# Kernel optimization log

Hardware: AMD Instinct MI355X
Metric: run time of the kernel (lower is better)

Reference implementation:

```python
import jax, jax.numpy as jnp
import numpy as np

N, E = 50000, 800000
IN, OUT = 128, 64  # in_channels, out_channels


def _w(key, fan_in, fan_out):
    return jax.random.normal(key, (fan_in, fan_out), dtype=jnp.float32) * (1.0 / np.sqrt(fan_in))


def setup_inputs() -> dict:
    key = jax.random.key(0)
    ks = jax.random.split(key, 16)
    x = jax.random.normal(ks[0], (N, IN), dtype=jnp.float32)
    edge_index = jax.random.randint(ks[1], (2, E), 0, N, dtype=jnp.int64)
    return {
        "x": x,
        "edge_index": edge_index,
        # Encoder: GCNConv(128->128), GCNConv(128->64), Linear(64->64)
        "ew1": _w(ks[2], IN, 2 * OUT), "eb1": jnp.zeros((2 * OUT,), jnp.float32),
        "ew2": _w(ks[3], 2 * OUT, OUT), "eb2": jnp.zeros((OUT,), jnp.float32),
        "efw": _w(ks[4], OUT, OUT), "efb": jnp.zeros((OUT,), jnp.float32),
        # Decoder: GCNConv(64->256), GCNConv(256->128), Linear(128->1024)
        "dw1": _w(ks[5], OUT, 2 * IN), "db1": jnp.zeros((2 * IN,), jnp.float32),
        "dw2": _w(ks[6], 2 * IN, IN), "db2": jnp.zeros((IN,), jnp.float32),
        "dfw": _w(ks[7], IN, 1024), "dfb": jnp.zeros((1024,), jnp.float32),
        # LinkPredictor: Linear(2*64 -> 1)
        "lw": _w(ks[8], 2 * OUT, 1), "lb": jnp.zeros((1,), jnp.float32),
    }


def gcn_conv(h_in, W, b, src, dst, dinv):
    # PyG GCNConv: linear transform, then symmetric-normalized aggregation
    # with implicit self-loops (deg includes the self-loop).
    h = h_in @ W  # [N, F_out]
    norm = (dinv[src] * dinv[dst])[:, None]      # per-edge symmetric norm
    agg = jax.ops.segment_sum(h[src] * norm, dst, num_segments=h.shape[0])
    agg = agg + h * (dinv * dinv)[:, None]       # self-loop contribution
    return agg + b


def reference(x, edge_index, ew1, eb1, ew2, eb2, efw, efb,
              dw1, db1, dw2, db2, dfw, dfb, lw, lb):
    src, dst = edge_index[0], edge_index[1]
    n = x.shape[0]
    # degree over A + I (self-loops added), computed on the target index
    deg = jax.ops.segment_sum(jnp.ones((src.shape[0],), x.dtype), dst,
                              num_segments=n) + 1.0
    dinv = deg ** -0.5

    # Encoder
    z = jax.nn.relu(gcn_conv(x, ew1, eb1, src, dst, dinv))
    z = gcn_conv(z, ew2, eb2, src, dst, dinv)
    z = z @ efw + efb  # latent [N, 64]

    # Decoder
    h = jax.nn.relu(gcn_conv(z, dw1, db1, src, dst, dinv))
    h = gcn_conv(h, dw2, db2, src, dst, dinv)
    x_hat = h @ dfw + dfb  # [N, 1024]

    # Link predictor on edge endpoint gathers
    zc = jnp.concatenate([z[src], z[dst]], axis=-1)  # [E, 128]
    edge_probs = jax.nn.sigmoid(zc @ lw + lb)        # [E, 1]
    return x_hat, edge_probs
```

## Files before the change

kernel.cpp:

```cpp
#include <hip/hip_runtime.h>
#include <hip/hip_bf16.h>

using bf16 = __hip_bfloat16;
typedef __attribute__((ext_vector_type(8))) short short8;
typedef __attribute__((ext_vector_type(4))) float f32x4;

static __device__ __forceinline__ float b2f(bf16 x) { return __bfloat162float(x); }

static __device__ __forceinline__ unsigned int packbf2(float a, float b) {
    bf16 x = __float2bfloat16(a), y = __float2bfloat16(b);
    unsigned short ux = *(unsigned short*)&x, uy = *(unsigned short*)&y;
    return (unsigned int)ux | ((unsigned int)uy << 16);
}

__global__ void det_kernel(const unsigned short* __restrict__ xh,
                           const int* __restrict__ ei, int* __restrict__ flags) {
    __shared__ int s_exp, s_nz;
    if (threadIdx.x == 0) { s_exp = 0; s_nz = 0; }
    __syncthreads();
    if (threadIdx.x < 256) {
        unsigned short h = xh[threadIdx.x];
        int ef = (h >> 7) & 0xFF;
        if (ef < 100 || ef > 140) atomicAdd(&s_exp, 1);
    }
    for (int i = 1 + 2 * threadIdx.x; i < 4096; i += 2 * blockDim.x)
        if (ei[i] != 0) atomicAdd(&s_nz, 1);
    __syncthreads();
    if (threadIdx.x == 0) {
        flags[0] = (s_exp > 16) ? 1 : 0;
        flags[1] = (s_nz == 0) ? 1 : 0;
    }
}

struct CanonWB { const void* src[8]; float* dst[8]; int n[8]; };

__global__ void canon_w_batch(CanonWB cb, const int* __restrict__ flags) {
    int j = blockIdx.x;
    const void* src = cb.src[j];
    float* dst = cb.dst[j];
    int n = cb.n[j];
    int m32 = flags[0];
    for (int i = threadIdx.x; i < n; i += blockDim.x)
        dst[i] = m32 ? ((const float*)src)[i] : b2f(((const bf16*)src)[i]);
}

__global__ void canon_x(const void* __restrict__ src, const int* __restrict__ flags,
                        bf16* __restrict__ dst, int n) {
    int i = blockIdx.x * blockDim.x + threadIdx.x;
    if (i >= n) return;
    dst[i] = flags[0] ? __float2bfloat16(((const float*)src)[i]) : ((const bf16*)src)[i];
}

__global__ void canon_edges_hist(const int* __restrict__ ei, const int* __restrict__ flags,
                                 int* __restrict__ srcd, int* __restrict__ dstd,
                                 int* __restrict__ counts, int E) {
    int e = blockIdx.x * blockDim.x + threadIdx.x;
    if (e >= E) return;
    int s, d;
    if (flags[1]) { s = ei[2 * e]; d = ei[2 * E + 2 * e]; }
    else          { s = ei[e];     d = ei[E + e]; }
    srcd[e] = s; dstd[e] = d;
    atomicAdd(&counts[d], 1);
}

struct PrepB { const void* src[6]; int lgK[6]; int F[6]; int off[6]; int end[6]; };

__global__ void prep_wt_batch(PrepB pb, const int* __restrict__ flags,
                              bf16* __restrict__ Wth, bf16* __restrict__ Wtl, int total) {
    int g = blockIdx.x * blockDim.x + threadIdx.x;
    if (g >= total) return;
    int j = 0;
#pragma unroll
    for (int t = 0; t < 6; ++t) if (g >= pb.end[t]) j = t + 1;
    const void* src = pb.src[j];
    int lgK = pb.lgK[j], F = pb.F[j];
    int local = g - pb.off[j];
    int f = local >> lgK, k = local & ((1 << lgK) - 1);
    float v = flags[0] ? ((const float*)src)[((size_t)k << 0) * F + (size_t)k * (F - 1) ? 0 : 0] : 0.0f;
    v = flags[0] ? ((const float*)src)[(size_t)k * F + f]
                 : b2f(((const bf16*)src)[(size_t)k * F + f]);
    bf16 hi = __float2bfloat16(v);
    float lo = v - b2f(hi);
    Wth[g] = hi;
    Wtl[g] = __float2bfloat16(lo);
}

__global__ void scan_part1(const int* __restrict__ counts, int* __restrict__ blockSums, int N) {
    __shared__ int red[256];
    int i = blockIdx.x * 256 + threadIdx.x;
    red[threadIdx.x] = (i < N) ? counts[i] : 0;
    __syncthreads();
    for (int off = 128; off > 0; off >>= 1) {
        if (threadIdx.x < off) red[threadIdx.x] += red[threadIdx.x + off];
        __syncthreads();
    }
    if (threadIdx.x == 0) blockSums[blockIdx.x] = red[0];
}

__global__ void scan_part2(const int* __restrict__ blockSums, int* __restrict__ blockOff,
                           int* __restrict__ rowPtrN, int G) {
    __shared__ int s[256];
    int t = threadIdx.x;
    s[t] = (t < G) ? blockSums[t] : 0;
    __syncthreads();
    for (int off = 1; off < 256; off <<= 1) {
        int v = (t >= off) ? s[t - off] : 0;
        __syncthreads();
        s[t] += v;
        __syncthreads();
    }
    if (t < G) blockOff[t] = (t > 0) ? s[t - 1] : 0;
    if (t == 255) *rowPtrN = s[255];
}

__global__ void scan_part3(const int* __restrict__ counts, const int* __restrict__ blockOff,
                           int* __restrict__ rowPtr, int* __restrict__ cursor,
                           float* __restrict__ dinv, int N) {
    __shared__ int s[256];
    int t = threadIdx.x;
    int i = blockIdx.x * 256 + t;
    int c = (i < N) ? counts[i] : 0;
    s[t] = c;
    __syncthreads();
    for (int off = 1; off < 256; off <<= 1) {
        int v = (t >= off) ? s[t - off] : 0;
        __syncthreads();
        s[t] += v;
        __syncthreads();
    }
    if (i < N) {
        int o = blockOff[blockIdx.x] + s[t] - c;
        rowPtr[i] = o;
        cursor[i] = o;
        dinv[i] = rsqrtf((float)c + 1.0f);
    }
}

__global__ void scatter_kernel(const int* __restrict__ srcv, const int* __restrict__ dstv,
                               int* __restrict__ cursor, int* __restrict__ sortedSrc, int E) {
    int e = blockIdx.x * blockDim.x + threadIdx.x;
    if (e >= E) return;
    int p = atomicAdd(&cursor[dstv[e]], 1);
    sortedSrc[p] = srcv[e];
}

template <int K>
__global__ __launch_bounds__(256)
void mfma_gemm(const bf16* __restrict__ A,
               const bf16* __restrict__ Wth, const bf16* __restrict__ Wtl,
               const float* __restrict__ bias, const float* __restrict__ dinv,
               void* __restrict__ out, const int* __restrict__ flags,
               int outmode, int relu, bf16* __restrict__ out2,
               const float* __restrict__ dinv2, int F, int N) {
    __shared__ uint4 lds4[1536];
    char* lds = (char*)lds4;
    const int tid = threadIdx.x;
    const int w = tid >> 6, lane = tid & 63;
    const int rowBase = blockIdx.y * 64;
    const int colBase = blockIdx.x * 64;

    f32x4 zero = {0.f, 0.f, 0.f, 0.f};
    f32x4 acc[4];
#pragma unroll
    for (int n = 0; n < 4; ++n) acc[n] = zero;

    const int arow = (w << 4) + (lane & 15);
    const int aswz = arow & 7;
    const int colL = lane & 15;

    for (int kc = 0; kc < K; kc += 64) {
#pragma unroll
        for (int i = 0; i < 6; ++i) {
            const int g = i * 256 + tid;
            char* dst = lds + ((i * 256 + (w << 6)) << 4);
            const bf16* src;
            if (g < 512) {
                int r = g >> 3, c = g & 7;
                int gr = rowBase + r; if (gr >= N) gr = N - 1;
                src = A + (size_t)gr * K + kc + ((c ^ (r & 7)) << 3);
            } else if (g < 1024) {
                int h = g - 512; int cl = h >> 3, c = h & 7;
                src = Wth + (size_t)(colBase + cl) * K + kc + ((c ^ (cl & 7)) << 3);
            } else {
                int h = g - 1024; int cl = h >> 3, c = h & 7;
                src = Wtl + (size_t)(colBase + cl) * K + kc + ((c ^ (cl & 7)) << 3);
            }
            __builtin_amdgcn_global_load_lds(
                (const __attribute__((address_space(1))) void*)src,
                (__attribute__((address_space(3))) void*)dst, 16, 0, 0);
        }
        __syncthreads();

        const char* aB = lds;
        const char* hB = lds + 8192;
        const char* lB = lds + 16384;
#pragma unroll
        for (int ks = 0; ks < 2; ++ks) {
            const int c = (ks << 2) + (lane >> 4);
            short8 a = *(const short8*)(aB + (((arow << 3) + (c ^ aswz)) << 4));
#pragma unroll
            for (int n = 0; n < 4; ++n) {
                const int col = (n << 4) + colL;
                const int s = ((col << 3) + (c ^ (col & 7))) << 4;
                short8 bh = *(const short8*)(hB + s);
                short8 bl = *(const short8*)(lB + s);
                acc[n] = __builtin_amdgcn_mfma_f32_16x16x32_bf16(a, bh, acc[n], 0, 0, 0);
                acc[n] = __builtin_amdgcn_mfma_f32_16x16x32_bf16(a, bl, acc[n], 0, 0, 0);
            }
        }
        __syncthreads();
    }

    const int m32 = outmode ? flags[0] : 0;
    const int r0 = rowBase + (w << 4) + ((lane >> 4) << 2);
#pragma unroll
    for (int n = 0; n < 4; ++n) {
        const int col = colBase + (n << 4) + colL;
        const float bv = bias ? bias[col] : 0.0f;
#pragma unroll
        for (int r = 0; r < 4; ++r) {
            const int row = r0 + r;
            if (row < N) {
                float v = acc[n][r];
                if (dinv) v *= dinv[row];
                v += bv;
                if (relu) v = fmaxf(v, 0.0f);
                size_t o = (size_t)row * F + col;
                if (m32) ((float*)out)[o] = v;
                else     ((bf16*)out)[o] = __float2bfloat16(v);
                if (out2) out2[o] = __float2bfloat16(v * dinv2[row]);
            }
        }
    }
}

template <int F>
static __device__ __forceinline__ void acc_row(const bf16* __restrict__ Hs, int row, int lane,
                                               float* acc) {
    if constexpr (F == 64) {
        unsigned short u = ((const unsigned short*)Hs)[(size_t)row * 64 + lane];
        union { unsigned int i; float f; } c; c.i = (unsigned int)u << 16;
        acc[0] += c.f;
    } else if constexpr (F == 128) {
        unsigned int u = ((const unsigned int*)(Hs + (size_t)row * 128))[lane];
        union { unsigned int i; float f; } lo, hi;
        lo.i = u << 16; hi.i = u & 0xffff0000u;
        acc[0] += lo.f; acc[1] += hi.f;
    } else {
        uint2 u = ((const uint2*)(Hs + (size_t)row * 256))[lane];
        union { unsigned int i; float f; } a, b, c, d;
        a.i = u.x << 16; b.i = u.x & 0xffff0000u;
        c.i = u.y << 16; d.i = u.y & 0xffff0000u;
        acc[0] += a.f; acc[1] += b.f; acc[2] += c.f; acc[3] += d.f;
    }
}

template <int F>
__global__ void gather_kernel(const bf16* __restrict__ Hs, const int* __restrict__ rowPtr,
                              const int* __restrict__ sortedSrc, const float* __restrict__ dinv,
                              const float* __restrict__ bias, bf16* __restrict__ out,
                              int relu, int N) {
    constexpr int WPL = F / 64;
    int node = blockIdx.x * (blockDim.x >> 6) + (threadIdx.x >> 6);
    int lane = threadIdx.x & 63;
    if (node >= N) return;
    float acc[WPL];
#pragma unroll
    for (int w = 0; w < WPL; ++w) acc[w] = 0.0f;
    acc_row<F>(Hs, node, lane, acc);
    const int beg = rowPtr[node], end = rowPtr[node + 1];
    for (int b = beg; b < end; b += 64) {
        int n = end - b; if (n > 64) n = 64;
        int myS = (lane < n) ? sortedSrc[b + lane] : 0;
        int j = 0;
        for (; j + 3 < n; j += 4) {
            int s0 = __shfl(myS, j),     s1 = __shfl(myS, j + 1);
            int s2 = __shfl(myS, j + 2), s3 = __shfl(myS, j + 3);
            acc_row<F>(Hs, s0, lane, acc);
            acc_row<F>(Hs, s1, lane, acc);
            acc_row<F>(Hs, s2, lane, acc);
            acc_row<F>(Hs, s3, lane, acc);
        }
        for (; j < n; ++j) acc_row<F>(Hs, __shfl(myS, j), lane, acc);
    }
    const float di = dinv[node];
    if constexpr (F == 64) {
        float v = acc[0] * di + (bias ? bias[lane] : 0.0f);
        if (relu) v = fmaxf(v, 0.0f);
        bf16 o = __float2bfloat16(v);
        ((unsigned short*)out)[(size_t)node * 64 + lane] = *(unsigned short*)&o;
    } else if constexpr (F == 128) {
        float b0 = bias ? bias[2 * lane] : 0.0f, b1 = bias ? bias[2 * lane + 1] : 0.0f;
        float v0 = acc[0] * di + b0;
        float v1 = acc[1] * di + b1;
        if (relu) { v0 = fmaxf(v0, 0.0f); v1 = fmaxf(v1, 0.0f); }
        ((unsigned int*)(out + (size_t)node * 128))[lane] = packbf2(v0, v1);
    } else {
        float v0 = acc[0] * di + (bias ? bias[4 * lane] : 0.0f);
        float v1 = acc[1] * di + (bias ? bias[4 * lane + 1] : 0.0f);
        float v2 = acc[2] * di + (bias ? bias[4 * lane + 2] : 0.0f);
        float v3 = acc[3] * di + (bias ? bias[4 * lane + 3] : 0.0f);
        if (relu) { v0 = fmaxf(v0, 0.0f); v1 = fmaxf(v1, 0.0f);
                    v2 = fmaxf(v2, 0.0f); v3 = fmaxf(v3, 0.0f); }
        uint2 p; p.x = packbf2(v0, v1); p.y = packbf2(v2, v3);
        ((uint2*)(out + (size_t)node * 256))[lane] = p;
    }
}

__global__ void link_pre(const bf16* __restrict__ Z, const float* __restrict__ lw,
                         float* __restrict__ ab, int N) {
    int node = blockIdx.x * (blockDim.x >> 6) + (threadIdx.x >> 6);
    int lane = threadIdx.x & 63;
    if (node >= N) return;
    float zv = b2f(Z[(size_t)node * 64 + lane]);
    float va = zv * lw[lane];
    float vb = zv * lw[64 + lane];
#pragma unroll
    for (int off = 32; off > 0; off >>= 1) {
        va += __shfl_down(va, off);
        vb += __shfl_down(vb, off);
    }
    if (lane == 0) { ab[2 * node] = va; ab[2 * node + 1] = vb; }
}

__global__ void link_edge(const float* __restrict__ ab, const int* __restrict__ srcv,
                          const int* __restrict__ dstv, const float* __restrict__ lb,
                          void* __restrict__ out, const int* __restrict__ flags,
                          size_t outOff, int E) {
    int e = blockIdx.x * blockDim.x + threadIdx.x;
    if (e >= E) return;
    float v = ab[2 * srcv[e]] + ab[2 * dstv[e] + 1] + lb[0];
    float sv = 1.0f / (1.0f + expf(-v));
    if (flags[0]) ((float*)out)[outOff + e] = sv;
    else          ((bf16*)out)[outOff + e] = __float2bfloat16(sv);
}

extern "C" void kernel_launch(void* const* d_in, const int* in_sizes, int n_in,
                              void* d_out, int out_size, void* d_ws, size_t ws_size,
                              hipStream_t stream) {
    const int N = in_sizes[0] / 128;
    const int E = in_sizes[1] / 2;

    char* base = (char*)d_ws;
    size_t off = 0;
    auto alloc = [&](size_t bytes) { char* p = base + off; off = (off + bytes + 255) & ~(size_t)255; return p; };
    int*   flags  = (int*)  alloc(256);
    float* dinv   = (float*)alloc((size_t)N * 4);
    float* Wc     = (float*)alloc((size_t)210689 * 4);
    int*   counts = (int*)  alloc((size_t)N * 4);
    int*   rowPtr = (int*)  alloc(((size_t)N + 1) * 4);
    int*   cursor = (int*)  alloc((size_t)N * 4);
    int*   sortedSrc = (int*)alloc((size_t)E * 4);
    int*   srcd   = (int*)  alloc((size_t)E * 4);
    int*   dstd   = (int*)  alloc((size_t)E * 4);
    bf16*  Hs     = (bf16*) alloc((size_t)N * 256 * 2);
    bf16*  P0     = (bf16*) alloc((size_t)N * 256 * 2);
    bf16*  z      = (bf16*) alloc((size_t)N * 64 * 2);
    bf16*  zs     = (bf16*) alloc((size_t)N * 64 * 2);
    bf16*  Wth    = (bf16*) alloc((size_t)208896 * 2);
    bf16*  Wtl    = (bf16*) alloc((size_t)208896 * 2);
    float* ab     = (float*)alloc((size_t)N * 2 * 4);
    int*   blockSums = (int*)alloc(256 * 4);
    int*   blockOff  = (int*)alloc(256 * 4);

    const int W_EB1 = 16384, W_EB2 = 24704, W_EFB = 28864, W_DB1 = 45312,
              W_DB2 = 78336, W_DFB = 209536, W_LW = 210560, W_LB = 210688;
    const int T_EW1 = 0, T_EW2 = 16384, T_EFW = 24576, T_DW1 = 28672,
              T_DW2 = 45056, T_DFW = 77824;

    det_kernel<<<1, 256, 0, stream>>>((const unsigned short*)d_in[0], (const int*)d_in[1], flags);

    hipMemsetAsync(counts, 0, (size_t)N * 4, stream);
    canon_edges_hist<<<(E + 255) / 256, 256, 0, stream>>>((const int*)d_in[1], flags,
                                                          srcd, dstd, counts, E);
    const int gScan = (N + 255) / 256;
    scan_part1<<<gScan, 256, 0, stream>>>(counts, blockSums, N);
    scan_part2<<<1, 256, 0, stream>>>(blockSums, blockOff, rowPtr + N, gScan);
    scan_part3<<<gScan, 256, 0, stream>>>(counts, blockOff, rowPtr, cursor, dinv, N);
    scatter_kernel<<<(E + 255) / 256, 256, 0, stream>>>(srcd, dstd, cursor, sortedSrc, E);

    {
        CanonWB cb;
        const int idx[8]  = {3, 5, 7, 9, 11, 13, 14, 15};
        const int woff[8] = {W_EB1, W_EB2, W_EFB, W_DB1, W_DB2, W_DFB, W_LW, W_LB};
        for (int j = 0; j < 8; ++j) {
            cb.src[j] = d_in[idx[j]];
            cb.dst[j] = Wc + woff[j];
            cb.n[j] = in_sizes[idx[j]];
        }
        canon_w_batch<<<8, 256, 0, stream>>>(cb, flags);
    }
    {
        PrepB pb;
        const int idx[6]  = {2, 4, 6, 8, 10, 12};
        const int toff[6] = {T_EW1, T_EW2, T_EFW, T_DW1, T_DW2, T_DFW};
        const int lgk[6]  = {7, 7, 6, 6, 8, 7};
        const int ff[6]   = {128, 64, 64, 256, 128, 1024};
        int total = 0;
        for (int j = 0; j < 6; ++j) {
            pb.src[j] = d_in[idx[j]];
            pb.lgK[j] = lgk[j];
            pb.F[j] = ff[j];
            pb.off[j] = toff[j];
            pb.end[j] = toff[j] + (ff[j] << lgk[j]);
            total = pb.end[j];
        }
        prep_wt_batch<<<(total + 255) / 256, 256, 0, stream>>>(pb, flags, Wth, Wtl, total);
    }
    canon_x<<<(N * 128 + 255) / 256, 256, 0, stream>>>(d_in[0], flags, P0, N * 128);

    const int gRB = (N + 63) / 64;
    const int gG = (N + 3) / 4;

    mfma_gemm<128><<<dim3(2, gRB), 256, 0, stream>>>(P0, Wth + T_EW1, Wtl + T_EW1,
                                                     nullptr, dinv, Hs, flags, 0, 0,
                                                     nullptr, nullptr, 128, N);
    gather_kernel<128><<<gG, 256, 0, stream>>>(Hs, rowPtr, sortedSrc, dinv, Wc + W_EB1, P0, 1, N);

    mfma_gemm<128><<<dim3(1, gRB), 256, 0, stream>>>(P0, Wth + T_EW2, Wtl + T_EW2,
                                                     nullptr, dinv, Hs, flags, 0, 0,
                                                     nullptr, nullptr, 64, N);
    gather_kernel<64><<<gG, 256, 0, stream>>>(Hs, rowPtr, sortedSrc, dinv, Wc + W_EB2, P0, 0, N);

    mfma_gemm<64><<<dim3(1, gRB), 256, 0, stream>>>(P0, Wth + T_EFW, Wtl + T_EFW,
                                                    Wc + W_EFB, nullptr, z, flags, 0, 0,
                                                    zs, dinv, 64, N);

    link_pre<<<gG, 256, 0, stream>>>(z, Wc + W_LW, ab, N);

    gather_kernel<64><<<gG, 256, 0, stream>>>(zs, rowPtr, sortedSrc, dinv, nullptr, Hs, 0, N);
    mfma_gemm<64><<<dim3(4, gRB), 256, 0, stream>>>(Hs, Wth + T_DW1, Wtl + T_DW1,
                                                    Wc + W_DB1, nullptr, P0, flags, 0, 1,
                                                    nullptr, nullptr, 256, N);

    mfma_gemm<256><<<dim3(2, gRB), 256, 0, stream>>>(P0, Wth + T_DW2, Wtl + T_DW2,
                                                     nullptr, dinv, Hs, flags, 0, 0,
                                                     nullptr, nullptr, 128, N);
    gather_kernel<128><<<gG, 256, 0, stream>>>(Hs, rowPtr, sortedSrc, dinv, Wc + W_DB2, P0, 0, N);

    mfma_gemm<128><<<dim3(16, gRB), 256, 0, stream>>>(P0, Wth + T_DFW, Wtl + T_DFW,
                                                      Wc + W_DFB, nullptr, d_out, flags, 1, 0,
                                                      nullptr, nullptr, 1024, N);

    link_edge<<<(E + 255) / 256, 256, 0, stream>>>(ab, srcd, dstd, Wc + W_LB,
                                                   d_out, flags, (size_t)N * 1024, E);
}
```

Before: 621.3 us.

## Split neighbor gather into half-wave dual-edge passes over 64-column slices

Replaces the templated per-F gather kernel with one kernel in which each half-wave handles a different edge and each lane loads 4 bytes (two bf16 columns) of a 64-column slice. The self-loop is folded into the index list, and the two halves are combined with a cross-half shuffle. 128-wide layers are now done as two launches over column slices, which is meant to give more memory requests in flight per wave and smaller per-pass working sets, at the cost of re-reading the CSR indices twice. It also vectorizes the input bf16 conversion to 8 elements per thread and removes a dead load in the weight prep.

```diff
diff --git a/kernel.cpp b/kernel.cpp
--- a/kernel.cpp
+++ b/kernel.cpp
@@ -44,11 +44,20 @@
         dst[i] = m32 ? ((const float*)src)[i] : b2f(((const bf16*)src)[i]);
 }
 
-__global__ void canon_x(const void* __restrict__ src, const int* __restrict__ flags,
-                        bf16* __restrict__ dst, int n) {
+__global__ void canon_x8(const void* __restrict__ src, const int* __restrict__ flags,
+                         bf16* __restrict__ dst, int n8) {
     int i = blockIdx.x * blockDim.x + threadIdx.x;
-    if (i >= n) return;
-    dst[i] = flags[0] ? __float2bfloat16(((const float*)src)[i]) : ((const bf16*)src)[i];
+    if (i >= n8) return;
+    if (flags[0]) {
+        const float4* s = (const float4*)src;
+        float4 x = s[2 * i], y = s[2 * i + 1];
+        uint4 r;
+        r.x = packbf2(x.x, x.y); r.y = packbf2(x.z, x.w);
+        r.z = packbf2(y.x, y.y); r.w = packbf2(y.z, y.w);
+        ((uint4*)dst)[i] = r;
+    } else {
+        ((uint4*)dst)[i] = ((const uint4*)src)[i];
+    }
 }
 
 __global__ void canon_edges_hist(const int* __restrict__ ei, const int* __restrict__ flags,
@@ -76,9 +85,8 @@
     int lgK = pb.lgK[j], F = pb.F[j];
     int local = g - pb.off[j];
     int f = local >> lgK, k = local & ((1 << lgK) - 1);
-    float v = flags[0] ? ((const float*)src)[((size_t)k << 0) * F + (size_t)k * (F - 1) ? 0 : 0] : 0.0f;
-    v = flags[0] ? ((const float*)src)[(size_t)k * F + f]
-                 : b2f(((const bf16*)src)[(size_t)k * F + f]);
+    float v = flags[0] ? ((const float*)src)[(size_t)k * F + f]
+                       : b2f(((const bf16*)src)[(size_t)k * F + f]);
     bf16 hi = __float2bfloat16(v);
     float lo = v - b2f(hi);
     Wth[g] = hi;
@@ -234,76 +242,53 @@
     }
 }
 
-template <int F>
-static __device__ __forceinline__ void acc_row(const bf16* __restrict__ Hs, int row, int lane,
-                                               float* acc) {
-    if constexpr (F == 64) {
-        unsigned short u = ((const unsigned short*)Hs)[(size_t)row * 64 + lane];
-        union { unsigned int i; float f; } c; c.i = (unsigned int)u << 16;
-        acc[0] += c.f;
-    } else if constexpr (F == 128) {
-        unsigned int u = ((const unsigned int*)(Hs + (size_t)row * 128))[lane];
-        union { unsigned int i; float f; } lo, hi;
-        lo.i = u << 16; hi.i = u & 0xffff0000u;
-        acc[0] += lo.f; acc[1] += hi.f;
-    } else {
-        uint2 u = ((const uint2*)(Hs + (size_t)row * 256))[lane];
-        union { unsigned int i; float f; } a, b, c, d;
-        a.i = u.x << 16; b.i = u.x & 0xffff0000u;
-        c.i = u.y << 16; d.i = u.y & 0xffff0000u;
-        acc[0] += a.f; acc[1] += b.f; acc[2] += c.f; acc[3] += d.f;
-    }
-}
-
-template <int F>
-__global__ void gather_kernel(const bf16* __restrict__ Hs, const int* __restrict__ rowPtr,
-                              const int* __restrict__ sortedSrc, const float* __restrict__ dinv,
-                              const float* __restrict__ bias, bf16* __restrict__ out,
-                              int relu, int N) {
-    constexpr int WPL = F / 64;
-    int node = blockIdx.x * (blockDim.x >> 6) + (threadIdx.x >> 6);
+__global__ void gather2(const bf16* __restrict__ Hs, const int* __restrict__ rowPtr,
+                        const int* __restrict__ sortedSrc, const float* __restrict__ dinv,
+                        const float* __restrict__ bias, bf16* __restrict__ out,
+                        int relu, int N, int stride, int colOff) {
+    int node = blockIdx.x * 4 + (threadIdx.x >> 6);
     int lane = threadIdx.x & 63;
     if (node >= N) return;
-    float acc[WPL];
-#pragma unroll
-    for (int w = 0; w < WPL; ++w) acc[w] = 0.0f;
-    acc_row<F>(Hs, node, lane, acc);
+    const int half = lane >> 5;
+    const int cl = lane & 31;
+    const size_t cbase = (size_t)colOff + 2 * cl;
+    float a0 = 0.0f, a1 = 0.0f;
     const int beg = rowPtr[node], end = rowPtr[node + 1];
-    for (int b = beg; b < end; b += 64) {
-        int n = end - b; if (n > 64) n = 64;
-        int myS = (lane < n) ? sortedSrc[b + lane] : 0;
+    const int total = end - beg + 1;
+    for (int b0 = 0; b0 < total; b0 += 64) {
+        int idx = b0 + lane;
+        int myS = 0;
+        if (idx == 0) myS = node;
+        else if (idx < total) myS = sortedSrc[beg + idx - 1];
+        int m = total - b0; if (m > 64) m = 64;
         int j = 0;
-        for (; j + 3 < n; j += 4) {
-            int s0 = __shfl(myS, j),     s1 = __shfl(myS, j + 1);
-            int s2 = __shfl(myS, j + 2), s3 = __shfl(myS, j + 3);
-            acc_row<F>(Hs, s0, lane, acc);
-            acc_row<F>(Hs, s1, lane, acc);
-            acc_row<F>(Hs, s2, lane, acc);
-            acc_row<F>(Hs, s3, lane, acc);
-        }
-        for (; j < n; ++j) acc_row<F>(Hs, __shfl(myS, j), lane, acc);
-    }
-    const float di = dinv[node];
-    if constexpr (F == 64) {
-        float v = acc[0] * di + (bias ? bias[lane] : 0.0f);
-        if (relu) v = fmaxf(v, 0.0f);
-        bf16 o = __float2bfloat16(v);
-        ((unsigned short*)out)[(size_t)node * 64 + lane] = *(unsigned short*)&o;
-    } else if constexpr (F == 128) {
-        float b0 = bias ? bias[2 * lane] : 0.0f, b1 = bias ? bias[2 * lane + 1] : 0.0f;
-        float v0 = acc[0] * di + b0;
-        float v1 = acc[1] * di + b1;
+        for (; j + 3 < m; j += 4) {
+            int s0 = __shfl(myS, j + half);
+            int s1 = __shfl(myS, j + 2 + half);
+            unsigned int u0 = *(const unsigned int*)(Hs + (size_t)s0 * stride + cbase);
+            unsigned int u1 = *(const unsigned int*)(Hs + (size_t)s1 * stride + cbase);
+            union { unsigned int i; float f; } lo, hi;
+            lo.i = u0 << 16; hi.i = u0 & 0xffff0000u; a0 += lo.f; a1 += hi.f;
+            lo.i = u1 << 16; hi.i = u1 & 0xffff0000u; a0 += lo.f; a1 += hi.f;
+        }
+        for (; j < m; j += 2) {
+            int idx2 = j + half;
+            int s0 = __shfl(myS, idx2);
+            if (idx2 < m) {
+                unsigned int u0 = *(const unsigned int*)(Hs + (size_t)s0 * stride + cbase);
+                union { unsigned int i; float f; } lo, hi;
+                lo.i = u0 << 16; hi.i = u0 & 0xffff0000u; a0 += lo.f; a1 += hi.f;
+            }
+        }
+    }
+    a0 += __shfl_xor(a0, 32);
+    a1 += __shfl_xor(a1, 32);
+    if (half == 0) {
+        const float di = dinv[node];
+        float v0 = a0 * di, v1 = a1 * di;
+        if (bias) { v0 += bias[cbase]; v1 += bias[cbase + 1]; }
         if (relu) { v0 = fmaxf(v0, 0.0f); v1 = fmaxf(v1, 0.0f); }
-        ((unsigned int*)(out + (size_t)node * 128))[lane] = packbf2(v0, v1);
-    } else {
-        float v0 = acc[0] * di + (bias ? bias[4 * lane] : 0.0f);
-        float v1 = acc[1] * di + (bias ? bias[4 * lane + 1] : 0.0f);
-        float v2 = acc[2] * di + (bias ? bias[4 * lane + 2] : 0.0f);
-        float v3 = acc[3] * di + (bias ? bias[4 * lane + 3] : 0.0f);
-        if (relu) { v0 = fmaxf(v0, 0.0f); v1 = fmaxf(v1, 0.0f);
-                    v2 = fmaxf(v2, 0.0f); v3 = fmaxf(v3, 0.0f); }
-        uint2 p; p.x = packbf2(v0, v1); p.y = packbf2(v2, v3);
-        ((uint2*)(out + (size_t)node * 256))[lane] = p;
+        *(unsigned int*)(out + (size_t)node * stride + cbase) = packbf2(v0, v1);
     }
 }
 
@@ -407,7 +392,7 @@
         }
         prep_wt_batch<<<(total + 255) / 256, 256, 0, stream>>>(pb, flags, Wth, Wtl, total);
     }
-    canon_x<<<(N * 128 + 255) / 256, 256, 0, stream>>>(d_in[0], flags, P0, N * 128);
+    canon_x8<<<(N * 16 + 255) / 256, 256, 0, stream>>>(d_in[0], flags, P0, N * 16);
 
     const int gRB = (N + 63) / 64;
     const int gG = (N + 3) / 4;
@@ -415,12 +400,13 @@
     mfma_gemm<128><<<dim3(2, gRB), 256, 0, stream>>>(P0, Wth + T_EW1, Wtl + T_EW1,
                                                      nullptr, dinv, Hs, flags, 0, 0,
                                                      nullptr, nullptr, 128, N);
-    gather_kernel<128><<<gG, 256, 0, stream>>>(Hs, rowPtr, sortedSrc, dinv, Wc + W_EB1, P0, 1, N);
+    gather2<<<gG, 256, 0, stream>>>(Hs, rowPtr, sortedSrc, dinv, Wc + W_EB1, P0, 1, N, 128, 0);
+    gather2<<<gG, 256, 0, stream>>>(Hs, rowPtr, sortedSrc, dinv, Wc + W_EB1, P0, 1, N, 128, 64);
 
     mfma_gemm<128><<<dim3(1, gRB), 256, 0, stream>>>(P0, Wth + T_EW2, Wtl + T_EW2,
                                                      nullptr, dinv, Hs, flags, 0, 0,
                                                      nullptr, nullptr, 64, N);
-    gather_kernel<64><<<gG, 256, 0, stream>>>(Hs, rowPtr, sortedSrc, dinv, Wc + W_EB2, P0, 0, N);
+    gather2<<<gG, 256, 0, stream>>>(Hs, rowPtr, sortedSrc, dinv, Wc + W_EB2, P0, 0, N, 64, 0);
 
     mfma_gemm<64><<<dim3(1, gRB), 256, 0, stream>>>(P0, Wth + T_EFW, Wtl + T_EFW,
                                                     Wc + W_EFB, nullptr, z, flags, 0, 0,
@@ -428,7 +414,7 @@
 
     link_pre<<<gG, 256, 0, stream>>>(z, Wc + W_LW, ab, N);
 
-    gather_kernel<64><<<gG, 256, 0, stream>>>(zs, rowPtr, sortedSrc, dinv, nullptr, Hs, 0, N);
+    gather2<<<gG, 256, 0, stream>>>(zs, rowPtr, sortedSrc, dinv, nullptr, Hs, 0, N, 64, 0);
     mfma_gemm<64><<<dim3(4, gRB), 256, 0, stream>>>(Hs, Wth + T_DW1, Wtl + T_DW1,
                                                     Wc + W_DB1, nullptr, P0, flags, 0, 1,
                                                     nullptr, nullptr, 256, N);
@@ -436,7 +422,8 @@
     mfma_gemm<256><<<dim3(2, gRB), 256, 0, stream>>>(P0, Wth + T_DW2, Wtl + T_DW2,
                                                      nullptr, dinv, Hs, flags, 0, 0,
                                                      nullptr, nullptr, 128, N);
-    gather_kernel<128><<<gG, 256, 0, stream>>>(Hs, rowPtr, sortedSrc, dinv, Wc + W_DB2, P0, 0, N);
+    gather2<<<gG, 256, 0, stream>>>(Hs, rowPtr, sortedSrc, dinv, Wc + W_DB2, P0, 0, N, 128, 0);
+    gather2<<<gG, 256, 0, stream>>>(Hs, rowPtr, sortedSrc, dinv, Wc + W_DB2, P0, 0, N, 128, 64);
 
     mfma_gemm<128><<<dim3(16, gRB), 256, 0, stream>>>(P0, Wth + T_DFW, Wtl + T_DFW,
                                                       Wc + W_DFB, nullptr, d_out, flags, 1, 0,
```

Measured after the change: 647.7 us. 4.2% more time.
